# Optimization experiments

Hardware: AMD Instinct MI355X
Metric: run time of the kernel (lower is better)

The kernel has to match this reference:

```python
import jax, jax.numpy as jnp
import numpy as np

N, E, D = 100_000, 1_250_000, 64
EPS = 1e-8

def setup_inputs() -> dict:
    key = jax.random.key(0)
    ks = jax.random.split(key, 8)
    h = jax.random.normal(ks[0], (N, D), jnp.float32)
    eig = jax.random.normal(ks[1], (E, 1), jnp.float32)          # per-edge vector field
    snorm_n = jax.random.uniform(ks[2], (N, 1), jnp.float32)     # node norm
    src = jax.random.randint(ks[3], (E,), 0, N)
    dst = jax.random.randint(ks[4], (E,), 0, N)
    # pretrans: Linear(2D -> D); posttrans: Linear((3+1)*D -> D); torch Linear weight is [out, in]
    W1 = jax.random.normal(ks[5], (D, 2 * D), jnp.float32) / np.sqrt(2.0 * D)
    b1 = jnp.zeros((D,), jnp.float32)
    W2 = jax.random.normal(ks[6], (D, 4 * D), jnp.float32) / np.sqrt(4.0 * D)
    b2 = jnp.zeros((D,), jnp.float32)
    gamma = jnp.ones((D,), jnp.float32)   # BatchNorm1d weight
    beta = jnp.zeros((D,), jnp.float32)   # BatchNorm1d bias
    return dict(h=h, eig=eig, snorm_n=snorm_n, src=src, dst=dst,
                W1=W1, b1=b1, W2=W2, b2=b2, gamma=gamma, beta=beta)

def reference(h, eig, snorm_n, src, dst, W1, b1, W2, b2, gamma, beta):
    seg = lambda x: jax.ops.segment_sum(x, dst, num_segments=N)
    # pretrans on edges: MLP(cat[h_src, h_dst])
    z2 = jnp.concatenate([h[src], h[dst]], axis=1)   # [E, 2D]
    e = z2 @ W1.T + b1                                # [E, D]
    deg = seg(jnp.ones((E, 1), e.dtype))              # [N, 1]
    # aggregator: mean
    agg_mean = seg(e) / jnp.maximum(deg, 1.0)
    # aggregator: max (empty segments -> 0)
    agg_max = jax.ops.segment_max(e, dst, num_segments=N)
    agg_max = jnp.where(deg > 0, agg_max, 0.0)
    # aggregator: directional derivative dir_dx
    absum = seg(jnp.abs(eig))                         # [N, 1] sum of |vf| per node
    w = eig / (absum[dst] + EPS)                      # [E, 1] normalized weights
    agg_dir = jnp.abs(seg(e * w) - seg(w) * h)        # [N, D]
    # posttrans on nodes
    hc = jnp.concatenate([h, agg_mean, agg_max, agg_dir], axis=1)  # [N, 4D]
    h2 = (hc @ W2.T + b2) * snorm_n
    # BatchNorm1d (training mode: batch stats, biased variance)
    mu = jnp.mean(h2, axis=0)
    var = jnp.var(h2, axis=0)
    h2 = (h2 - mu) * jax.lax.rsqrt(var + 1e-5) * gamma + beta
    h2 = jax.nn.relu(h2)
    # residual (in_dim == out_dim); dropout p=0 is identity
    return h + h2
```

## Files before the change

kernel.cpp:

```cpp
#include <hip/hip_runtime.h>
#include <math.h>

__device__ __forceinline__ float bf2f(unsigned short s) {
    return __uint_as_float(((unsigned)s) << 16);
}
__device__ __forceinline__ unsigned short f2bf(float f) {
    unsigned u = __float_as_uint(f);
    unsigned r = (u + 0x7fffu + ((u >> 16) & 1u)) >> 16;
    return (unsigned short)r;
}

typedef __attribute__((ext_vector_type(8))) short short8v;
typedef __attribute__((ext_vector_type(4))) float f32x4;


__device__ __forceinline__ void edge_rank_body(
    int bid, const int* __restrict__ dst, int* __restrict__ cursor,
    int* __restrict__ rank, int E)
{
    int t = bid * 256 + threadIdx.x;
    int base = t * 8;
    if (base >= E) return;
    if (base + 8 <= E) {
        int4 d0 = *(const int4*)(dst + base);
        int4 d1 = *(const int4*)(dst + base + 4);
        int r0 = atomicAdd(&cursor[d0.x], 1);
        int r1 = atomicAdd(&cursor[d0.y], 1);
        int r2 = atomicAdd(&cursor[d0.z], 1);
        int r3 = atomicAdd(&cursor[d0.w], 1);
        int r4 = atomicAdd(&cursor[d1.x], 1);
        int r5 = atomicAdd(&cursor[d1.y], 1);
        int r6 = atomicAdd(&cursor[d1.z], 1);
        int r7 = atomicAdd(&cursor[d1.w], 1);
        *(int4*)(rank + base)     = make_int4(r0, r1, r2, r3);
        *(int4*)(rank + base + 4) = make_int4(r4, r5, r6, r7);
    } else {
        for (int e = base; e < E; ++e)
            rank[e] = atomicAdd(&cursor[dst[e]], 1);
    }
}

__device__ __forceinline__ void hb_cast_body(
    int bid, const float* __restrict__ h, unsigned short* __restrict__ hb, long total8)
{
    long idx = (long)bid * 256 + threadIdx.x;
    if (idx >= total8) return;
    const float4 a = *(const float4*)(h + idx * 8);
    const float4 b = *(const float4*)(h + idx * 8 + 4);
    union { unsigned short s[8]; uint4 v4; } pk;
    pk.s[0] = f2bf(a.x); pk.s[1] = f2bf(a.y); pk.s[2] = f2bf(a.z); pk.s[3] = f2bf(a.w);
    pk.s[4] = f2bf(b.x); pk.s[5] = f2bf(b.y); pk.s[6] = f2bf(b.z); pk.s[7] = f2bf(b.w);
    *(uint4*)(hb + idx * 8) = pk.v4;
}

__device__ __forceinline__ void wprep_body(
    int bid, const float* __restrict__ W1, const float* __restrict__ W2,
    unsigned short* __restrict__ w1bf, unsigned short* __restrict__ w2bf)
{
    int idx = bid * 256 + threadIdx.x;
    if (idx < 128 * 64) {
        int c = idx >> 6, j = idx & 63;
        float val = (c < 64) ? W1[c * 128 + j] : W1[(c - 64) * 128 + 64 + j];
        w1bf[idx] = f2bf(val);
    } else if (idx < 128 * 64 + 64 * 256) {
        int k = idx - 128 * 64;
        w2bf[k] = f2bf(W2[k]);
    }
}

__device__ __forceinline__ void csr_scatter_body(
    int bid, const int* __restrict__ src, const int* __restrict__ dst,
    const float* __restrict__ eig, const int* __restrict__ rank,
    const int* __restrict__ offs, int2* __restrict__ csr, int E)
{
    int e = bid * 256 + threadIdx.x;
    if (e < E) {
        int dn = dst[e];
        int p = offs[dn] + rank[e];
        csr[p] = make_int2(src[e], __float_as_int(eig[e]));
    }
}

__device__ __forceinline__ void uv_mfma_body(
    int bid, const unsigned short* __restrict__ hb, const unsigned short* __restrict__ w1bf,
    const float* __restrict__ b1,
    unsigned short* __restrict__ u, unsigned short* __restrict__ v)
{
    int lane = threadIdx.x & 63;
    int wv = threadIdx.x >> 6;
    int lr = lane & 15;
    int lg = lane >> 4;

    short8v a[2][2];
#pragma unroll
    for (int rt = 0; rt < 2; ++rt)
#pragma unroll
        for (int s = 0; s < 2; ++s)
            a[rt][s] = *(const short8v*)(w1bf + (size_t)(wv * 32 + rt * 16 + lr) * 64 + s * 32 + lg * 8);

    float b1v[2][4];
#pragma unroll
    for (int rt = 0; rt < 2; ++rt) {
        if (wv >= 2) {
            float4 t4 = *(const float4*)(b1 + (wv - 2) * 32 + rt * 16 + lg * 4);
            b1v[rt][0] = t4.x; b1v[rt][1] = t4.y; b1v[rt][2] = t4.z; b1v[rt][3] = t4.w;
        } else {
            b1v[rt][0] = b1v[rt][1] = b1v[rt][2] = b1v[rt][3] = 0.f;
        }
    }

    unsigned short* outp = (wv < 2) ? u : v;
    int coff0 = (wv & 1) * 32 + lg * 4;

    int n0 = bid * 64;

    short8v bb[2][2];
    {
        const unsigned short* hp = hb + (size_t)(n0 + lr) * 64 + lg * 8;
        bb[0][0] = *(const short8v*)(hp);
        bb[0][1] = *(const short8v*)(hp + 32);
    }
#pragma unroll
    for (int t = 0; t < 4; ++t) {
        int cur = t & 1, nxt = cur ^ 1;
        if (t < 3) {
            const unsigned short* hp = hb + (size_t)(n0 + (t + 1) * 16 + lr) * 64 + lg * 8;
            bb[nxt][0] = *(const short8v*)(hp);
            bb[nxt][1] = *(const short8v*)(hp + 32);
        }
        f32x4 acc0 = {0.f, 0.f, 0.f, 0.f}, acc1 = {0.f, 0.f, 0.f, 0.f};
        acc0 = __builtin_amdgcn_mfma_f32_16x16x32_bf16(a[0][0], bb[cur][0], acc0, 0, 0, 0);
        acc1 = __builtin_amdgcn_mfma_f32_16x16x32_bf16(a[1][0], bb[cur][0], acc1, 0, 0, 0);
        acc0 = __builtin_amdgcn_mfma_f32_16x16x32_bf16(a[0][1], bb[cur][1], acc0, 0, 0, 0);
        acc1 = __builtin_amdgcn_mfma_f32_16x16x32_bf16(a[1][1], bb[cur][1], acc1, 0, 0, 0);
        int node = n0 + t * 16 + lr;
        union { unsigned short s[4]; uint2 v2; } pk;
#pragma unroll
        for (int r = 0; r < 4; ++r) pk.s[r] = f2bf(acc0[r] + b1v[0][r]);
        *(uint2*)(outp + (size_t)node * 64 + coff0) = pk.v2;
#pragma unroll
        for (int r = 0; r < 4; ++r) pk.s[r] = f2bf(acc1[r] + b1v[1][r]);
        *(uint2*)(outp + (size_t)node * 64 + coff0 + 16) = pk.v2;
    }
}

__global__ __launch_bounds__(256) void mega1_kernel(
    const int* __restrict__ dst, int* __restrict__ cursor, int* __restrict__ rank, int E,
    const float* __restrict__ h, unsigned short* __restrict__ hb, long total8,
    const float* __restrict__ W1, const float* __restrict__ W2,
    unsigned short* __restrict__ w1bf, unsigned short* __restrict__ w2bf,
    int nrank, int ncast)
{
    int b = blockIdx.x;
    if (b < nrank)              edge_rank_body(b, dst, cursor, rank, E);
    else if (b < nrank + ncast) hb_cast_body(b - nrank, h, hb, total8);
    else                        wprep_body(b - nrank - ncast, W1, W2, w1bf, w2bf);
}

__global__ __launch_bounds__(256) void mega2_kernel(
    const unsigned short* __restrict__ hb, const unsigned short* __restrict__ w1bf,
    const float* __restrict__ b1, unsigned short* __restrict__ u, unsigned short* __restrict__ v,
    const int* __restrict__ src, const int* __restrict__ dst, const float* __restrict__ eig,
    const int* __restrict__ rank, const int* __restrict__ offs, int2* __restrict__ csr,
    int E, int nuv)
{
    int b = blockIdx.x;
    if (b < nuv) uv_mfma_body(b, hb, w1bf, b1, u, v);
    else         csr_scatter_body(b - nuv, src, dst, eig, rank, offs, csr, E);
}

__global__ __launch_bounds__(256) void block_reduce_kernel(
    const int* __restrict__ deg, int* __restrict__ bsum, int N)
{
    __shared__ int sd[256];
    int t = threadIdx.x;
    int i = blockIdx.x * 256 + t;
    sd[t] = (i < N) ? deg[i] : 0;
    __syncthreads();
    for (int s = 128; s > 0; s >>= 1) {
        if (t < s) sd[t] += sd[t + s];
        __syncthreads();
    }
    if (t == 0) bsum[blockIdx.x] = sd[0];
}

__global__ __launch_bounds__(1024) void scan_bsums_kernel(
    const int* __restrict__ bsum, int* __restrict__ bscan, int nb)
{
    __shared__ int sd[1024];
    int t = threadIdx.x;
    int own = (t < nb) ? bsum[t] : 0;
    sd[t] = own;
    __syncthreads();
    for (int off = 1; off < 1024; off <<= 1) {
        int v = (t >= off) ? sd[t - off] : 0;
        __syncthreads();
        sd[t] += v;
        __syncthreads();
    }
    if (t < nb) bscan[t] = sd[t] - own;
}

__global__ __launch_bounds__(256) void block_scan_kernel(
    const int* __restrict__ deg, const int* __restrict__ bscan,
    int* __restrict__ offs, int N)
{
    __shared__ int sd[256];
    int t = threadIdx.x;
    int i = blockIdx.x * 256 + t;
    int myv = (i < N) ? deg[i] : 0;
    sd[t] = myv;
    __syncthreads();
    for (int off = 1; off < 256; off <<= 1) {
        int v = (t >= off) ? sd[t - off] : 0;
        __syncthreads();
        sd[t] += v;
        __syncthreads();
    }
    if (i < N) {
        offs[i] = sd[t] - myv + bscan[blockIdx.x];
    }
}

__global__ __launch_bounds__(256) void agg_kernel(
    const unsigned short* __restrict__ u, const unsigned short* __restrict__ v,
    const unsigned short* __restrict__ hb,
    const int* __restrict__ offs, const int* __restrict__ degi,
    const int2* __restrict__ csr,
    unsigned short* __restrict__ agg, int N)
{
    int gw = (blockIdx.x * 256 + threadIdx.x) >> 6;
    int lane = threadIdx.x & 63;
    int n = __builtin_amdgcn_readfirstlane(gw);
    if (n >= N) return;
    int dn  = __builtin_amdgcn_readfirstlane(degi[n]);
    int beg = __builtin_amdgcn_readfirstlane(offs[n]);

    float vl = bf2f(v[(size_t)n * 64 + lane]);
    float hl = bf2f(hb[(size_t)n * 64 + lane]);

    const int2* ep = csr + beg;
    float accs = 0.f, accd = 0.f, accm = -3.402823466e38f;
    float pa = 0.f, ps = 0.f;

    int j = 0;
    for (; j + 4 <= dn; j += 4) {
        int2 r0 = ep[j], r1 = ep[j + 1], r2 = ep[j + 2], r3 = ep[j + 3];
        float u0 = bf2f(u[(size_t)r0.x * 64 + lane]);
        float u1 = bf2f(u[(size_t)r1.x * 64 + lane]);
        float u2 = bf2f(u[(size_t)r2.x * 64 + lane]);
        float u3 = bf2f(u[(size_t)r3.x * 64 + lane]);
        float w0 = __int_as_float(r0.y), w1 = __int_as_float(r1.y);
        float w2_ = __int_as_float(r2.y), w3 = __int_as_float(r3.y);
        pa += (fabsf(w0) + fabsf(w1)) + (fabsf(w2_) + fabsf(w3));
        ps += (w0 + w1) + (w2_ + w3);
        accs += (u0 + u1) + (u2 + u3);
        accm = fmaxf(accm, fmaxf(fmaxf(u0, u1), fmaxf(u2, u3)));
        accd = fmaf(w0, u0, fmaf(w1, u1, fmaf(w2_, u2, fmaf(w3, u3, accd))));
    }
    for (; j < dn; ++j) {
        int2 r0 = ep[j];
        float u0 = bf2f(u[(size_t)r0.x * 64 + lane]);
        float w0 = __int_as_float(r0.y);
        pa += fabsf(w0);
        ps += w0;
        accs += u0;
        accm = fmaxf(accm, u0);
        accd = fmaf(w0, u0, accd);
    }

    float inv_ab = 1.f / (pa + 1e-8f);
    float segw = ps * inv_ab;

    float fdeg = (float)dn;
    float mean = (accs + fdeg * vl) / fmaxf(fdeg, 1.f);
    float amax = (dn > 0) ? (accm + vl) : 0.f;
    float adir = fabsf(fmaf(accd, inv_ab, segw * (vl - hl)));
    size_t base = (size_t)n * 192;
    agg[base + lane]       = f2bf(mean);
    agg[base + 64 + lane]  = f2bf(amax);
    agg[base + 128 + lane] = f2bf(adir);
}

__global__ __launch_bounds__(256) void post_mfma_kernel(
    const unsigned short* __restrict__ hb, const unsigned short* __restrict__ agg,
    const unsigned short* __restrict__ w2bf, const float* __restrict__ b2,
    const float* __restrict__ snorm, float* __restrict__ h2,
    float* __restrict__ bn_part, int N)
{
    int lane = threadIdx.x & 63;
    int w = threadIdx.x >> 6;
    int lr = lane & 15;
    int lg = lane >> 4;

    short8v a[8];
    {
        const unsigned short* ab = w2bf + ((size_t)(w * 16 + lr)) * 256 + lg * 8;
#pragma unroll
        for (int s = 0; s < 8; ++s)
            a[s] = *(const short8v*)(ab + s * 32);
    }
    float4 b2v = *(const float4*)(b2 + w * 16 + lg * 4);
    float b2a[4] = {b2v.x, b2v.y, b2v.z, b2v.w};

    int n0 = blockIdx.x * 128;
    float s1[4] = {0.f, 0.f, 0.f, 0.f}, s2[4] = {0.f, 0.f, 0.f, 0.f};

    short8v bb[2][8];
    float snv[2];

#define LOADT(BUF, T)                                                            \
    {                                                                            \
        int node_ = n0 + (T) * 16 + lr;                                          \
        const unsigned short* hbp_ = hb  + (size_t)node_ * 64  + lg * 8;         \
        const unsigned short* agp_ = agg + (size_t)node_ * 192 + lg * 8;         \
        bb[BUF][0] = *(const short8v*)(hbp_);                                    \
        bb[BUF][1] = *(const short8v*)(hbp_ + 32);                               \
        bb[BUF][2] = *(const short8v*)(agp_);                                    \
        bb[BUF][3] = *(const short8v*)(agp_ + 32);                               \
        bb[BUF][4] = *(const short8v*)(agp_ + 64);                               \
        bb[BUF][5] = *(const short8v*)(agp_ + 96);                               \
        bb[BUF][6] = *(const short8v*)(agp_ + 128);                              \
        bb[BUF][7] = *(const short8v*)(agp_ + 160);                              \
        int nc_ = (node_ < N) ? node_ : (N - 1);                                 \
        snv[BUF] = snorm[nc_];                                                   \
    }

    LOADT(0, 0)
#pragma unroll
    for (int t = 0; t < 8; ++t) {
        int cur = t & 1, nxt = cur ^ 1;
        if (t < 7) LOADT(nxt, t + 1)
        f32x4 acc0 = {0.f, 0.f, 0.f, 0.f}, acc1 = {0.f, 0.f, 0.f, 0.f};
#pragma unroll
        for (int s = 0; s < 8; s += 2) {
            acc0 = __builtin_amdgcn_mfma_f32_16x16x32_bf16(a[s],     bb[cur][s],     acc0, 0, 0, 0);
            acc1 = __builtin_amdgcn_mfma_f32_16x16x32_bf16(a[s + 1], bb[cur][s + 1], acc1, 0, 0, 0);
        }
        int node = n0 + t * 16 + lr;
        bool ok = node < N;
        float sn = snv[cur];
        float xr[4];
#pragma unroll
        for (int r = 0; r < 4; ++r) {
            float val = (acc0[r] + acc1[r] + b2a[r]) * sn;
            val = ok ? val : 0.f;
            xr[r] = val;
            s1[r] += val;
            s2[r] = fmaf(val, val, s2[r]);
        }
        *(float4*)(h2 + (size_t)node * 64 + w * 16 + lg * 4) =
            make_float4(xr[0], xr[1], xr[2], xr[3]);
    }
#undef LOADT

#pragma unroll
    for (int m = 1; m < 16; m <<= 1) {
#pragma unroll
        for (int r = 0; r < 4; ++r) {
            s1[r] += __shfl_xor(s1[r], m);
            s2[r] += __shfl_xor(s2[r], m);
        }
    }
    if (lr == 0) {
        int d = w * 16 + lg * 4;
        float* bp = bn_part + (size_t)blockIdx.x * 128;
#pragma unroll
        for (int r = 0; r < 4; ++r) {
            bp[d + r]      = s1[r];
            bp[64 + d + r] = s2[r];
        }
    }
}

__global__ __launch_bounds__(1024) void bn_reduce_kernel(
    const float* __restrict__ bn_part, const float* __restrict__ gamma,
    const float* __restrict__ beta, float* __restrict__ bn_buf, int nblk, float invN)
{
    __shared__ float sred[1024];
    int t = threadIdx.x;
    int d = t & 127;
    int sl = t >> 7;
    float s = 0.f;
    for (int b = sl; b < nblk; b += 8)
        s += bn_part[(size_t)b * 128 + d];
    sred[t] = s;
    __syncthreads();
    if (sl == 0) {
        float tot = s;
#pragma unroll
        for (int k = 1; k < 8; ++k) tot += sred[k * 128 + d];
        sred[d] = tot;
    }
    __syncthreads();
    if (t < 64) {
        float s1 = sred[t], s2 = sred[64 + t];
        float mu = s1 * invN;
        float var = s2 * invN - mu * mu;
        float rstd = rsqrtf(var + 1e-5f);
        float sc = rstd * gamma[t];
        bn_buf[t]      = sc;
        bn_buf[64 + t] = beta[t] - mu * sc;
    }
}

__global__ __launch_bounds__(256) void bn_final_kernel(
    const float* __restrict__ h, const float* __restrict__ h2,
    const float* __restrict__ bn_buf, float* __restrict__ out, int N)
{
    int idx = blockIdx.x * 256 + threadIdx.x;
    int total4 = N * 16;
    if (idx >= total4) return;
    int base = idx * 4;
    int d0 = base & 63;
    const float4 a = *(const float4*)(h2 + base);
    const float4 hh = *(const float4*)(h + base);
    float r[4] = {a.x, a.y, a.z, a.w};
    float hv[4] = {hh.x, hh.y, hh.z, hh.w};
    float o[4];
#pragma unroll
    for (int k = 0; k < 4; ++k) {
        int d = d0 + k;
        float x = fmaf(r[k], bn_buf[d], bn_buf[64 + d]);
        o[k] = hv[k] + fmaxf(x, 0.f);
    }
    float4 ov = {o[0], o[1], o[2], o[3]};
    *(float4*)(out + base) = ov;
}

extern "C" void kernel_launch(void* const* d_in, const int* in_sizes, int n_in,
                              void* d_out, int out_size, void* d_ws, size_t ws_size,
                              hipStream_t stream)
{
    const float* h     = (const float*)d_in[0];
    const float* eig   = (const float*)d_in[1];
    const float* snorm = (const float*)d_in[2];
    const int*   src   = (const int*)d_in[3];
    const int*   dst   = (const int*)d_in[4];
    const float* W1    = (const float*)d_in[5];
    const float* b1    = (const float*)d_in[6];
    const float* W2    = (const float*)d_in[7];
    const float* b2    = (const float*)d_in[8];
    const float* gamma = (const float*)d_in[9];
    const float* beta  = (const float*)d_in[10];
    float* out = (float*)d_out;

    const int N = in_sizes[2];
    const int E = in_sizes[1];
    const int Npad = (N + 255) & ~255;
    const int pblk = (N + 127) / 128;

    char* w = (char*)d_ws;
    size_t off = 0;
    auto alloc = [&](size_t bytes) -> char* {
        char* p = w + off;
        off += (bytes + 255) & ~size_t(255);
        return p;
    };
    unsigned short* u = (unsigned short*)alloc((size_t)Npad * 64 * 2);
    unsigned short* v = (unsigned short*)alloc((size_t)Npad * 64 * 2);
    float* h2 = (float*)u;
    unsigned short* agg = (unsigned short*)alloc((size_t)Npad * 192 * 2);
    unsigned short* hb  = (unsigned short*)alloc((size_t)Npad * 64 * 2);
    int2* csr = (int2*)alloc((size_t)E * 8);
    int*  rank = (int*)alloc((size_t)E * 4);
    char* zero_base = w + off;
    int*   cursor = (int*)alloc((size_t)N * 4);
    size_t zero_bytes = (size_t)((w + off) - zero_base);
    float* bn_part = (float*)alloc((size_t)pblk * 128 * 4);
    float* bn_buf  = (float*)alloc(128 * 4);
    int* offs = (int*)alloc((size_t)N * 4);
    int nb = (N + 255) / 256;
    int* bsum  = (int*)alloc((size_t)nb * 4);
    int* bscan = (int*)alloc((size_t)nb * 4);
    unsigned short* w1bf = (unsigned short*)alloc(128 * 64 * 2);
    unsigned short* w2bf = (unsigned short*)alloc(64 * 256 * 2);
    (void)ws_size; (void)n_in; (void)out_size;

    hipMemsetAsync(zero_base, 0, zero_bytes, stream);

    long total8 = (long)N * 8;
    int nrank = (E + 2047) / 2048;
    int ncast = (int)((total8 + 255) / 256);
    int nwprep = (128 * 64 + 64 * 256 + 255) / 256;
    mega1_kernel<<<nrank + ncast + nwprep, 256, 0, stream>>>(
        dst, cursor, rank, E, h, hb, total8, W1, W2, w1bf, w2bf, nrank, ncast);

    block_reduce_kernel<<<nb, 256, 0, stream>>>(cursor, bsum, N);
    scan_bsums_kernel<<<1, 1024, 0, stream>>>(bsum, bscan, nb);
    block_scan_kernel<<<nb, 256, 0, stream>>>(cursor, bscan, offs, N);

    int nuv = (N + 63) / 64;
    int nscat = (E + 255) / 256;
    mega2_kernel<<<nuv + nscat, 256, 0, stream>>>(
        hb, w1bf, b1, u, v, src, dst, eig, rank, offs, csr, E, nuv);

    int agrid = (int)(((size_t)N * 64 + 255) / 256);
    agg_kernel<<<agrid, 256, 0, stream>>>(u, v, hb, offs, cursor, csr, agg, N);

    post_mfma_kernel<<<pblk, 256, 0, stream>>>(hb, agg, w2bf, b2, snorm,
                                               h2, bn_part, N);

    bn_reduce_kernel<<<1, 1024, 0, stream>>>(bn_part, gamma, beta, bn_buf, pblk, 1.0f / (float)N);

    int fgrid = (N * 16 + 255) / 256;
    bn_final_kernel<<<fgrid, 256, 0, stream>>>(h, h2, bn_buf, out, N);
}
```

Baseline: 317.9 us.

## Convert weights to bf16 inline, unroll aggregation by 8, halve post-GEMM block size

Drops the separate weight-prep pass: the uv and post-transform MFMA kernels now read fp32 W1/W2 directly and pack them to bf16 in registers. The aggregation loop gains an 8-edge unrolled path so more neighbour gathers are in flight at once. The post-transform kernel processes 64 nodes per block instead of 128, which doubles the grid and the number of BN partial sums. Each block now repeats the weight conversion, and the extra unrolling raises register pressure.

```diff
diff --git a/kernel.cpp b/kernel.cpp
--- a/kernel.cpp
+++ b/kernel.cpp
@@ -12,6 +12,15 @@
 
 typedef __attribute__((ext_vector_type(8))) short short8v;
 typedef __attribute__((ext_vector_type(4))) float f32x4;
+
+__device__ __forceinline__ short8v pack8(float4 a, float4 b) {
+    short8v r;
+    r[0] = (short)f2bf(a.x); r[1] = (short)f2bf(a.y);
+    r[2] = (short)f2bf(a.z); r[3] = (short)f2bf(a.w);
+    r[4] = (short)f2bf(b.x); r[5] = (short)f2bf(b.y);
+    r[6] = (short)f2bf(b.z); r[7] = (short)f2bf(b.w);
+    return r;
+}
 
 
 __device__ __forceinline__ void edge_rank_body(
@@ -53,21 +62,6 @@
     *(uint4*)(hb + idx * 8) = pk.v4;
 }
 
-__device__ __forceinline__ void wprep_body(
-    int bid, const float* __restrict__ W1, const float* __restrict__ W2,
-    unsigned short* __restrict__ w1bf, unsigned short* __restrict__ w2bf)
-{
-    int idx = bid * 256 + threadIdx.x;
-    if (idx < 128 * 64) {
-        int c = idx >> 6, j = idx & 63;
-        float val = (c < 64) ? W1[c * 128 + j] : W1[(c - 64) * 128 + 64 + j];
-        w1bf[idx] = f2bf(val);
-    } else if (idx < 128 * 64 + 64 * 256) {
-        int k = idx - 128 * 64;
-        w2bf[k] = f2bf(W2[k]);
-    }
-}
-
 __device__ __forceinline__ void csr_scatter_body(
     int bid, const int* __restrict__ src, const int* __restrict__ dst,
     const float* __restrict__ eig, const int* __restrict__ rank,
@@ -82,7 +76,7 @@
 }
 
 __device__ __forceinline__ void uv_mfma_body(
-    int bid, const unsigned short* __restrict__ hb, const unsigned short* __restrict__ w1bf,
+    int bid, const unsigned short* __restrict__ hb, const float* __restrict__ W1,
     const float* __restrict__ b1,
     unsigned short* __restrict__ u, unsigned short* __restrict__ v)
 {
@@ -93,10 +87,17 @@
 
     short8v a[2][2];
 #pragma unroll
-    for (int rt = 0; rt < 2; ++rt)
-#pragma unroll
-        for (int s = 0; s < 2; ++s)
-            a[rt][s] = *(const short8v*)(w1bf + (size_t)(wv * 32 + rt * 16 + lr) * 64 + s * 32 + lg * 8);
+    for (int rt = 0; rt < 2; ++rt) {
+        int c = wv * 32 + rt * 16 + lr;
+        const float* wp = (c < 64) ? (W1 + (size_t)c * 128)
+                                   : (W1 + (size_t)(c - 64) * 128 + 64);
+#pragma unroll
+        for (int s = 0; s < 2; ++s) {
+            float4 q0 = *(const float4*)(wp + s * 32 + lg * 8);
+            float4 q1 = *(const float4*)(wp + s * 32 + lg * 8 + 4);
+            a[rt][s] = pack8(q0, q1);
+        }
+    }
 
     float b1v[2][4];
 #pragma unroll
@@ -147,25 +148,22 @@
 __global__ __launch_bounds__(256) void mega1_kernel(
     const int* __restrict__ dst, int* __restrict__ cursor, int* __restrict__ rank, int E,
     const float* __restrict__ h, unsigned short* __restrict__ hb, long total8,
-    const float* __restrict__ W1, const float* __restrict__ W2,
-    unsigned short* __restrict__ w1bf, unsigned short* __restrict__ w2bf,
-    int nrank, int ncast)
+    int nrank)
 {
     int b = blockIdx.x;
-    if (b < nrank)              edge_rank_body(b, dst, cursor, rank, E);
-    else if (b < nrank + ncast) hb_cast_body(b - nrank, h, hb, total8);
-    else                        wprep_body(b - nrank - ncast, W1, W2, w1bf, w2bf);
+    if (b < nrank) edge_rank_body(b, dst, cursor, rank, E);
+    else           hb_cast_body(b - nrank, h, hb, total8);
 }
 
 __global__ __launch_bounds__(256) void mega2_kernel(
-    const unsigned short* __restrict__ hb, const unsigned short* __restrict__ w1bf,
+    const unsigned short* __restrict__ hb, const float* __restrict__ W1,
     const float* __restrict__ b1, unsigned short* __restrict__ u, unsigned short* __restrict__ v,
     const int* __restrict__ src, const int* __restrict__ dst, const float* __restrict__ eig,
     const int* __restrict__ rank, const int* __restrict__ offs, int2* __restrict__ csr,
     int E, int nuv)
 {
     int b = blockIdx.x;
-    if (b < nuv) uv_mfma_body(b, hb, w1bf, b1, u, v);
+    if (b < nuv) uv_mfma_body(b, hb, W1, b1, u, v);
     else         csr_scatter_body(b - nuv, src, dst, eig, rank, offs, csr, E);
 }
 
@@ -244,6 +242,30 @@
     float pa = 0.f, ps = 0.f;
 
     int j = 0;
+    for (; j + 8 <= dn; j += 8) {
+        int2 r0 = ep[j],     r1 = ep[j + 1], r2 = ep[j + 2], r3 = ep[j + 3];
+        int2 r4 = ep[j + 4], r5 = ep[j + 5], r6 = ep[j + 6], r7 = ep[j + 7];
+        float u0 = bf2f(u[(size_t)r0.x * 64 + lane]);
+        float u1 = bf2f(u[(size_t)r1.x * 64 + lane]);
+        float u2 = bf2f(u[(size_t)r2.x * 64 + lane]);
+        float u3 = bf2f(u[(size_t)r3.x * 64 + lane]);
+        float u4 = bf2f(u[(size_t)r4.x * 64 + lane]);
+        float u5 = bf2f(u[(size_t)r5.x * 64 + lane]);
+        float u6 = bf2f(u[(size_t)r6.x * 64 + lane]);
+        float u7 = bf2f(u[(size_t)r7.x * 64 + lane]);
+        float w0 = __int_as_float(r0.y), w1 = __int_as_float(r1.y);
+        float w2_ = __int_as_float(r2.y), w3 = __int_as_float(r3.y);
+        float w4 = __int_as_float(r4.y), w5 = __int_as_float(r5.y);
+        float w6 = __int_as_float(r6.y), w7 = __int_as_float(r7.y);
+        pa += ((fabsf(w0) + fabsf(w1)) + (fabsf(w2_) + fabsf(w3)))
+            + ((fabsf(w4) + fabsf(w5)) + (fabsf(w6) + fabsf(w7)));
+        ps += ((w0 + w1) + (w2_ + w3)) + ((w4 + w5) + (w6 + w7));
+        accs += ((u0 + u1) + (u2 + u3)) + ((u4 + u5) + (u6 + u7));
+        accm = fmaxf(accm, fmaxf(fmaxf(fmaxf(u0, u1), fmaxf(u2, u3)),
+                                 fmaxf(fmaxf(u4, u5), fmaxf(u6, u7))));
+        accd = fmaf(w0, u0, fmaf(w1, u1, fmaf(w2_, u2, fmaf(w3, u3, accd))));
+        accd = fmaf(w4, u4, fmaf(w5, u5, fmaf(w6, u6, fmaf(w7, u7, accd))));
+    }
     for (; j + 4 <= dn; j += 4) {
         int2 r0 = ep[j], r1 = ep[j + 1], r2 = ep[j + 2], r3 = ep[j + 3];
         float u0 = bf2f(u[(size_t)r0.x * 64 + lane]);
@@ -284,7 +306,7 @@
 
 __global__ __launch_bounds__(256) void post_mfma_kernel(
     const unsigned short* __restrict__ hb, const unsigned short* __restrict__ agg,
-    const unsigned short* __restrict__ w2bf, const float* __restrict__ b2,
+    const float* __restrict__ W2, const float* __restrict__ b2,
     const float* __restrict__ snorm, float* __restrict__ h2,
     float* __restrict__ bn_part, int N)
 {
@@ -295,15 +317,19 @@
 
     short8v a[8];
     {
-        const unsigned short* ab = w2bf + ((size_t)(w * 16 + lr)) * 256 + lg * 8;
-#pragma unroll
-        for (int s = 0; s < 8; ++s)
-            a[s] = *(const short8v*)(ab + s * 32);
+        int d = w * 16 + lr;
+        const float* wp = W2 + (size_t)d * 256 + lg * 8;
+#pragma unroll
+        for (int s = 0; s < 8; ++s) {
+            float4 q0 = *(const float4*)(wp + s * 32);
+            float4 q1 = *(const float4*)(wp + s * 32 + 4);
+            a[s] = pack8(q0, q1);
+        }
     }
     float4 b2v = *(const float4*)(b2 + w * 16 + lg * 4);
     float b2a[4] = {b2v.x, b2v.y, b2v.z, b2v.w};
 
-    int n0 = blockIdx.x * 128;
+    int n0 = blockIdx.x * 64;
     float s1[4] = {0.f, 0.f, 0.f, 0.f}, s2[4] = {0.f, 0.f, 0.f, 0.f};
 
     short8v bb[2][8];
@@ -328,9 +354,9 @@
 
     LOADT(0, 0)
 #pragma unroll
-    for (int t = 0; t < 8; ++t) {
+    for (int t = 0; t < 4; ++t) {
         int cur = t & 1, nxt = cur ^ 1;
-        if (t < 7) LOADT(nxt, t + 1)
+        if (t < 3) LOADT(nxt, t + 1)
         f32x4 acc0 = {0.f, 0.f, 0.f, 0.f}, acc1 = {0.f, 0.f, 0.f, 0.f};
 #pragma unroll
         for (int s = 0; s < 8; s += 2) {
@@ -448,7 +474,7 @@
     const int N = in_sizes[2];
     const int E = in_sizes[1];
     const int Npad = (N + 255) & ~255;
-    const int pblk = (N + 127) / 128;
+    const int pblk = (N + 63) / 64;
 
     char* w = (char*)d_ws;
     size_t off = 0;
@@ -473,8 +499,6 @@
     int nb = (N + 255) / 256;
     int* bsum  = (int*)alloc((size_t)nb * 4);
     int* bscan = (int*)alloc((size_t)nb * 4);
-    unsigned short* w1bf = (unsigned short*)alloc(128 * 64 * 2);
-    unsigned short* w2bf = (unsigned short*)alloc(64 * 256 * 2);
     (void)ws_size; (void)n_in; (void)out_size;
 
     hipMemsetAsync(zero_base, 0, zero_bytes, stream);
@@ -482,9 +506,8 @@
     long total8 = (long)N * 8;
     int nrank = (E + 2047) / 2048;
     int ncast = (int)((total8 + 255) / 256);
-    int nwprep = (128 * 64 + 64 * 256 + 255) / 256;
-    mega1_kernel<<<nrank + ncast + nwprep, 256, 0, stream>>>(
-        dst, cursor, rank, E, h, hb, total8, W1, W2, w1bf, w2bf, nrank, ncast);
+    mega1_kernel<<<nrank + ncast, 256, 0, stream>>>(
+        dst, cursor, rank, E, h, hb, total8, nrank);
 
     block_reduce_kernel<<<nb, 256, 0, stream>>>(cursor, bsum, N);
     scan_bsums_kernel<<<1, 1024, 0, stream>>>(bsum, bscan, nb);
@@ -493,12 +516,12 @@
     int nuv = (N + 63) / 64;
     int nscat = (E + 255) / 256;
     mega2_kernel<<<nuv + nscat, 256, 0, stream>>>(
-        hb, w1bf, b1, u, v, src, dst, eig, rank, offs, csr, E, nuv);
+        hb, W1, b1, u, v, src, dst, eig, rank, offs, csr, E, nuv);
 
     int agrid = (int)(((size_t)N * 64 + 255) / 256);
     agg_kernel<<<agrid, 256, 0, stream>>>(u, v, hb, offs, cursor, csr, agg, N);
 
-    post_mfma_kernel<<<pblk, 256, 0, stream>>>(hb, agg, w2bf, b2, snorm,
+    post_mfma_kernel<<<pblk, 256, 0, stream>>>(hb, agg, W2, b2, snorm,
                                                h2, bn_part, N);
 
     bn_reduce_kernel<<<1, 1024, 0, stream>>>(bn_part, gamma, beta, bn_buf, pblk, 1.0f / (float)N);
```

New measurement: 356.0 us. +12.0%, slower.
